# Kernel tuning notes

Hardware: AMD Instinct MI355X
Metric: run time of the kernel (lower is better)

The kernel has to match this reference:

```python
import jax, jax.numpy as jnp
import numpy as np

B, F, U, G = 2048, 512, 512, 64
REG_STRENGTH = 1.0


def setup_inputs() -> dict:
    key = jax.random.key(0)
    k0, k1, k2, k3, k4 = jax.random.split(key, 5)
    x = jax.random.normal(k0, (B, F), dtype=jnp.float32)
    gid = jax.random.randint(k1, (B,), 0, G, dtype=jnp.int64)
    # glorot-normal-ish scale for kernels: sqrt(2/(fan_in+fan_out))
    glorot = np.sqrt(2.0 / (U + F)).astype(np.float32)
    w_mu = jax.random.normal(k2, (G, U, F), dtype=jnp.float32) * glorot
    b_mu = jax.random.normal(k3, (G, U), dtype=jnp.float32) * 0.05  # 'random_normal' init
    w0_mu = jax.random.normal(k4, (U, F), dtype=jnp.float32) * glorot
    b0_mu = jnp.zeros((U,), dtype=jnp.float32)
    return {"x": x, "gid": gid, "w_mu": w_mu, "b_mu": b_mu, "w0_mu": w0_mu, "b0_mu": b0_mu}


def reference(x, gid, w_mu, b_mu, w0_mu, b0_mu):
    # Hard top-1 routing: per-sample weight matrix gather, [B, U, F]
    w = jnp.take(w_mu, gid, axis=0)
    b = jnp.take(b_mu, gid, axis=0)  # [B, U]
    # Batched matvec: 'Bup,Bp->Bu'
    outputs = jnp.einsum("buf,bf->bu", w, x) + b  # use_bias=True, activation=None
    # L2 prior regularization loss (added via add_loss in the original)
    w_loss = jnp.sum(jnp.square(w - w0_mu[None]))  # sum over axes [1,2] then batch
    b_loss = jnp.sum(jnp.square(b - b0_mu[None]))
    reg_loss = REG_STRENGTH * (w_loss + b_loss)
    return outputs, reg_loss
```

## Files before the change

kernel.cpp:

```cpp
#include <hip/hip_runtime.h>

#define B_SZ 2048
#define F_SZ 512
#define U_SZ 512
#define G_SZ 64
#define REG_STRENGTH 1.0f

#define NT 8
#define BN 64
#define BK 64
#define NSTEP (F_SZ / BK)
#define MROWS 64
#define THREADS 256
#define NBLOCKS (NT * G_SZ)

typedef float f32x4 __attribute__((ext_vector_type(4)));
typedef __bf16 bf16x8 __attribute__((ext_vector_type(8)));

#define MFMA(a, b, c) __builtin_amdgcn_mfma_f32_16x16x32_bf16((a), (b), (c), 0, 0, 0)

static __device__ __forceinline__ unsigned short bf16_rne(float f) {
  unsigned u = __float_as_uint(f);
  return (unsigned short)((u + 0x7fffu + ((u >> 16) & 1u)) >> 16);
}

static __device__ __forceinline__ void cvt8(const f32x4 a, const f32x4 b,
                                            bf16x8& h, bf16x8& l) {
#pragma unroll
  for (int i = 0; i < 4; ++i) {
    const unsigned short hb = bf16_rne(a[i]);
    h[i] = __builtin_bit_cast(__bf16, hb);
    l[i] = __builtin_bit_cast(
        __bf16, bf16_rne(a[i] - __uint_as_float((unsigned)hb << 16)));
  }
#pragma unroll
  for (int i = 0; i < 4; ++i) {
    const unsigned short hb = bf16_rne(b[i]);
    h[4 + i] = __builtin_bit_cast(__bf16, hb);
    l[4 + i] = __builtin_bit_cast(
        __bf16, bf16_rne(b[i] - __uint_as_float((unsigned)hb << 16)));
  }
}

static __device__ __forceinline__ void writeX(unsigned short* __restrict__ xh,
                                              unsigned short* __restrict__ xl,
                                              int row, int kq, const f32x4 v) {
  int byte = (row << 7) + (kq << 3);
  byte ^= (row & 7) << 4;
  const unsigned short h0 = bf16_rne(v[0]);
  const unsigned short h1 = bf16_rne(v[1]);
  const unsigned short h2 = bf16_rne(v[2]);
  const unsigned short h3 = bf16_rne(v[3]);
  const ushort4 hv = make_ushort4(h0, h1, h2, h3);
  const ushort4 lv = make_ushort4(
      bf16_rne(v[0] - __uint_as_float((unsigned)h0 << 16)),
      bf16_rne(v[1] - __uint_as_float((unsigned)h1 << 16)),
      bf16_rne(v[2] - __uint_as_float((unsigned)h2 << 16)),
      bf16_rne(v[3] - __uint_as_float((unsigned)h3 << 16)));
  *(ushort4*)((char*)xh + byte) = hv;
  *(ushort4*)((char*)xl + byte) = lv;
}

static __device__ __forceinline__ bf16x8 readA(
    const unsigned short* __restrict__ base, int m, int kk, int llo, int lhi) {
  const int row = (m << 4) + llo;
  int byte = (row << 7) + (kk << 6) + (lhi << 4);
  byte ^= (row & 7) << 4;
  return *(const bf16x8*)((const char*)base + byte);
}

__global__ __launch_bounds__(THREADS, 2) void fused_kernel(
    const float* __restrict__ x, const int* __restrict__ gid,
    const float* __restrict__ w_mu, const float* __restrict__ b_mu,
    const float* __restrict__ w0_mu, const float* __restrict__ b0_mu,
    float* __restrict__ out, float* __restrict__ wsf,
    unsigned* __restrict__ done) {
  __shared__ __align__(16) unsigned short XH[2][MROWS * BK];
  __shared__ __align__(16) unsigned short XL[2][MROWS * BK];
  __shared__ int rows_s[B_SZ];
  __shared__ int cnt_s;
  __shared__ float red_s[THREADS / 64];

  const int f = blockIdx.x;
  const int r8 = f & 7;
  const int q = f >> 3;
  const int nt = q & 7;
  const int g = ((q >> 3) << 3) + r8;

  const int tid = threadIdx.x;
  const int lane = tid & 63;
  const int wv = tid >> 6;
  const int lhi = lane >> 4;
  const int llo = lane & 15;

  if (tid == 0) cnt_s = 0;
  __syncthreads();
#pragma unroll
  for (int u = 0; u < 2; ++u) {
    const int4 v = ((const int4*)gid)[tid + u * THREADS];
    const int b0 = (tid + u * THREADS) << 2;
    if (v.x == g) rows_s[atomicAdd(&cnt_s, 1)] = b0;
    if (v.y == g) rows_s[atomicAdd(&cnt_s, 1)] = b0 + 1;
    if (v.z == g) rows_s[atomicAdd(&cnt_s, 1)] = b0 + 2;
    if (v.w == g) rows_s[atomicAdd(&cnt_s, 1)] = b0 + 3;
  }
  __syncthreads();
  const int cnt = cnt_s;

  if (cnt > 0) {
    const int mycol = nt * BN + wv * 16 + llo;
    const float* __restrict__ wrow =
        w_mu + (size_t)g * (U_SZ * F_SZ) + (size_t)mycol * F_SZ;
    const float* __restrict__ w0row = w0_mu + (size_t)mycol * F_SZ;

    float regp = 0.0f;
    if (nt == 0) {
      for (int u = tid; u < U_SZ; u += THREADS) {
        const float d = b_mu[(g << 9) + u] - b0_mu[u];
        regp += d * d;
      }
    }

    for (int r0c = 0; r0c < cnt; r0c += MROWS) {
      const int rc = min(MROWS, cnt - r0c);
      const int nf4 = rc << 4;
      const int mt = (rc + 15) >> 4;
      const bool doreg = (r0c == 0);
      f32x4 acc[4];
#pragma unroll
      for (int m = 0; m < 4; ++m) acc[m] = (f32x4){0.f, 0.f, 0.f, 0.f};

#pragma unroll
      for (int u = 0; u < 4; ++u) {
        const int i = tid + u * THREADS;
        if (i < nf4) {
          const int row = i >> 4, kq = i & 15;
          const f32x4 v = *(const f32x4*)(
              x + (size_t)rows_s[r0c + row] * F_SZ + (kq << 2));
          writeX(&XH[0][0], &XL[0][0], row, kq, v);
        }
      }
      __syncthreads();

      for (int s = 0; s < NSTEP; ++s) {
        const int buf = s & 1;
        f32x4 xr[4];
        if (s + 1 < NSTEP) {
          const int kc = (s + 1) * BK;
#pragma unroll
          for (int u = 0; u < 4; ++u) {
            const int i = tid + u * THREADS;
            if (i < nf4) {
              const int row = i >> 4, kq = i & 15;
              xr[u] = *(const f32x4*)(
                  x + (size_t)rows_s[r0c + row] * F_SZ + kc + (kq << 2));
            }
          }
        }
        const int kcs = s * BK + (lhi << 3);
        const f32x4 wa0 = *(const f32x4*)(wrow + kcs);
        const f32x4 wa1 = *(const f32x4*)(wrow + kcs + 4);
        const f32x4 wb0 = *(const f32x4*)(wrow + kcs + 32);
        const f32x4 wb1 = *(const f32x4*)(wrow + kcs + 32 + 4);
        if (doreg) {
          const f32x4 z0 = *(const f32x4*)(w0row + kcs);
          const f32x4 z1 = *(const f32x4*)(w0row + kcs + 4);
          const f32x4 z2 = *(const f32x4*)(w0row + kcs + 32);
          const f32x4 z3 = *(const f32x4*)(w0row + kcs + 32 + 4);
#pragma unroll
          for (int i = 0; i < 4; ++i) {
            const float d0 = wa0[i] - z0[i], d1 = wa1[i] - z1[i];
            const float d2 = wb0[i] - z2[i], d3 = wb1[i] - z3[i];
            regp += d0 * d0 + d1 * d1 + d2 * d2 + d3 * d3;
          }
        }
        bf16x8 wh0, wl0, wh1, wl1;
        cvt8(wa0, wa1, wh0, wl0);
        cvt8(wb0, wb1, wh1, wl1);
#pragma unroll
        for (int m = 0; m < 4; ++m) {
          if (m < mt) {
            const bf16x8 ah0 = readA(&XH[buf][0], m, 0, llo, lhi);
            const bf16x8 al0 = readA(&XL[buf][0], m, 0, llo, lhi);
            acc[m] = MFMA(ah0, wh0, acc[m]);
            acc[m] = MFMA(ah0, wl0, acc[m]);
            acc[m] = MFMA(al0, wh0, acc[m]);
            const bf16x8 ah1 = readA(&XH[buf][0], m, 1, llo, lhi);
            const bf16x8 al1 = readA(&XL[buf][0], m, 1, llo, lhi);
            acc[m] = MFMA(ah1, wh1, acc[m]);
            acc[m] = MFMA(ah1, wl1, acc[m]);
            acc[m] = MFMA(al1, wh1, acc[m]);
          }
        }
        if (s + 1 < NSTEP) {
#pragma unroll
          for (int u = 0; u < 4; ++u) {
            const int i = tid + u * THREADS;
            if (i < nf4) {
              const int row = i >> 4, kq = i & 15;
              writeX(&XH[buf ^ 1][0], &XL[buf ^ 1][0], row, kq, xr[u]);
            }
          }
        }
        __syncthreads();
      }

      const float bias = b_mu[(g << 9) + mycol];
#pragma unroll
      for (int m = 0; m < 4; ++m) {
        if (m < mt) {
#pragma unroll
          for (int j = 0; j < 4; ++j) {
            const int rl = (m << 4) + (lhi << 2) + j;
            if (rl < rc) {
              out[(size_t)rows_s[r0c + rl] * U_SZ + mycol] = acc[m][j] + bias;
            }
          }
        }
      }
    }

#pragma unroll
    for (int o = 32; o > 0; o >>= 1) regp += __shfl_down(regp, o, 64);
    if (lane == 0) red_s[wv] = regp;
    __syncthreads();
    if (tid == 0) {
      atomicAdd(wsf, (float)cnt * (red_s[0] + red_s[1] + red_s[2] + red_s[3]));
    }
  }

  if (tid == 0) {
    __threadfence();
    const unsigned prev = atomicAdd(done, 1u);
    if (prev == (unsigned)(gridDim.x - 1)) {
      __threadfence();
      const float v = atomicAdd(wsf, 0.0f);
      out[(size_t)B_SZ * U_SZ] = REG_STRENGTH * v;
    }
  }
}

extern "C" void kernel_launch(void* const* d_in, const int* in_sizes, int n_in,
                              void* d_out, int out_size, void* d_ws,
                              size_t ws_size, hipStream_t stream) {
  (void)in_sizes; (void)n_in; (void)out_size; (void)ws_size;
  const float* x     = (const float*)d_in[0];
  const int*   gid   = (const int*)d_in[1];
  const float* w_mu  = (const float*)d_in[2];
  const float* b_mu  = (const float*)d_in[3];
  const float* w0_mu = (const float*)d_in[4];
  const float* b0_mu = (const float*)d_in[5];

  float* wsf = (float*)d_ws;
  unsigned* done = (unsigned*)d_ws + 1;

  hipMemsetAsync(d_ws, 0, 8, stream);
  fused_kernel<<<NBLOCKS, THREADS, 0, stream>>>(x, gid, w_mu, b_mu, w0_mu,
                                                b0_mu, (float*)d_out, wsf, done);
}
```

Baseline: 146.0 us.

## Drop LDS staging of x; load activations straight from global per wave

Removes the double-buffered shared-memory staging of the x rows and the block-wide barriers. Each wave now loads its own x fragments directly from global memory and converts them to split bf16 in registers. Conversions use native __bf16 casts instead of manual rounding. The final reduction moves to per-wave atomics with a wave-level completion counter. This cuts LDS traffic and synchronization, but every wave reloads and reconverts the same x rows, so redundant global loads and conversion work increase.

New measurement: 192.9 us. +32.1%, slower.

```diff
diff --git a/kernel.cpp b/kernel.cpp
--- a/kernel.cpp
+++ b/kernel.cpp
@@ -7,66 +7,29 @@
 #define REG_STRENGTH 1.0f
 
 #define NT 8
-#define BN 64
-#define BK 64
-#define NSTEP (F_SZ / BK)
-#define MROWS 64
 #define THREADS 256
 #define NBLOCKS (NT * G_SZ)
+#define NWAVES (NBLOCKS * 4)
 
 typedef float f32x4 __attribute__((ext_vector_type(4)));
 typedef __bf16 bf16x8 __attribute__((ext_vector_type(8)));
 
 #define MFMA(a, b, c) __builtin_amdgcn_mfma_f32_16x16x32_bf16((a), (b), (c), 0, 0, 0)
 
-static __device__ __forceinline__ unsigned short bf16_rne(float f) {
-  unsigned u = __float_as_uint(f);
-  return (unsigned short)((u + 0x7fffu + ((u >> 16) & 1u)) >> 16);
-}
-
 static __device__ __forceinline__ void cvt8(const f32x4 a, const f32x4 b,
                                             bf16x8& h, bf16x8& l) {
 #pragma unroll
   for (int i = 0; i < 4; ++i) {
-    const unsigned short hb = bf16_rne(a[i]);
-    h[i] = __builtin_bit_cast(__bf16, hb);
-    l[i] = __builtin_bit_cast(
-        __bf16, bf16_rne(a[i] - __uint_as_float((unsigned)hb << 16)));
+    const __bf16 hb = (__bf16)a[i];
+    h[i] = hb;
+    l[i] = (__bf16)(a[i] - (float)hb);
   }
 #pragma unroll
   for (int i = 0; i < 4; ++i) {
-    const unsigned short hb = bf16_rne(b[i]);
-    h[4 + i] = __builtin_bit_cast(__bf16, hb);
-    l[4 + i] = __builtin_bit_cast(
-        __bf16, bf16_rne(b[i] - __uint_as_float((unsigned)hb << 16)));
+    const __bf16 hb = (__bf16)b[i];
+    h[4 + i] = hb;
+    l[4 + i] = (__bf16)(b[i] - (float)hb);
   }
-}
-
-static __device__ __forceinline__ void writeX(unsigned short* __restrict__ xh,
-                                              unsigned short* __restrict__ xl,
-                                              int row, int kq, const f32x4 v) {
-  int byte = (row << 7) + (kq << 3);
-  byte ^= (row & 7) << 4;
-  const unsigned short h0 = bf16_rne(v[0]);
-  const unsigned short h1 = bf16_rne(v[1]);
-  const unsigned short h2 = bf16_rne(v[2]);
-  const unsigned short h3 = bf16_rne(v[3]);
-  const ushort4 hv = make_ushort4(h0, h1, h2, h3);
-  const ushort4 lv = make_ushort4(
-      bf16_rne(v[0] - __uint_as_float((unsigned)h0 << 16)),
-      bf16_rne(v[1] - __uint_as_float((unsigned)h1 << 16)),
-      bf16_rne(v[2] - __uint_as_float((unsigned)h2 << 16)),
-      bf16_rne(v[3] - __uint_as_float((unsigned)h3 << 16)));
-  *(ushort4*)((char*)xh + byte) = hv;
-  *(ushort4*)((char*)xl + byte) = lv;
-}
-
-static __device__ __forceinline__ bf16x8 readA(
-    const unsigned short* __restrict__ base, int m, int kk, int llo, int lhi) {
-  const int row = (m << 4) + llo;
-  int byte = (row << 7) + (kk << 6) + (lhi << 4);
-  byte ^= (row & 7) << 4;
-  return *(const bf16x8*)((const char*)base + byte);
 }
 
 __global__ __launch_bounds__(THREADS, 2) void fused_kernel(
@@ -75,11 +38,8 @@
     const float* __restrict__ w0_mu, const float* __restrict__ b0_mu,
     float* __restrict__ out, float* __restrict__ wsf,
     unsigned* __restrict__ done) {
-  __shared__ __align__(16) unsigned short XH[2][MROWS * BK];
-  __shared__ __align__(16) unsigned short XL[2][MROWS * BK];
   __shared__ int rows_s[B_SZ];
   __shared__ int cnt_s;
-  __shared__ float red_s[THREADS / 64];
 
   const int f = blockIdx.x;
   const int r8 = f & 7;
@@ -108,10 +68,10 @@
   const int cnt = cnt_s;
 
   if (cnt > 0) {
-    const int mycol = nt * BN + wv * 16 + llo;
-    const float* __restrict__ wrow =
-        w_mu + (size_t)g * (U_SZ * F_SZ) + (size_t)mycol * F_SZ;
-    const float* __restrict__ w0row = w0_mu + (size_t)mycol * F_SZ;
+    const int mycol = nt * 64 + wv * 16 + llo;
+    const float* __restrict__ wp =
+        w_mu + (size_t)g * (U_SZ * F_SZ) + (size_t)mycol * F_SZ + (lhi << 3);
+    const float* __restrict__ w0p = w0_mu + (size_t)mycol * F_SZ + (lhi << 3);
 
     float regp = 0.0f;
     if (nt == 0) {
@@ -121,88 +81,50 @@
       }
     }
 
-    for (int r0c = 0; r0c < cnt; r0c += MROWS) {
-      const int rc = min(MROWS, cnt - r0c);
-      const int nf4 = rc << 4;
+    for (int r0c = 0; r0c < cnt; r0c += 64) {
+      const int rc = min(64, cnt - r0c);
       const int mt = (rc + 15) >> 4;
       const bool doreg = (r0c == 0);
+
+      const float* xp[4];
+#pragma unroll
+      for (int m = 0; m < 4; ++m) {
+        int r = r0c + (m << 4) + llo;
+        if (r >= cnt) r = cnt - 1;
+        xp[m] = x + (size_t)rows_s[r] * F_SZ + (lhi << 3);
+      }
+
       f32x4 acc[4];
 #pragma unroll
       for (int m = 0; m < 4; ++m) acc[m] = (f32x4){0.f, 0.f, 0.f, 0.f};
 
+#pragma unroll 4
+      for (int kc = 0; kc < F_SZ; kc += 32) {
+        const f32x4 wa = *(const f32x4*)(wp + kc);
+        const f32x4 wb = *(const f32x4*)(wp + kc + 4);
+        if (doreg) {
+          const f32x4 za = *(const f32x4*)(w0p + kc);
+          const f32x4 zb = *(const f32x4*)(w0p + kc + 4);
 #pragma unroll
-      for (int u = 0; u < 4; ++u) {
-        const int i = tid + u * THREADS;
-        if (i < nf4) {
-          const int row = i >> 4, kq = i & 15;
-          const f32x4 v = *(const f32x4*)(
-              x + (size_t)rows_s[r0c + row] * F_SZ + (kq << 2));
-          writeX(&XH[0][0], &XL[0][0], row, kq, v);
-        }
-      }
-      __syncthreads();
-
-      for (int s = 0; s < NSTEP; ++s) {
-        const int buf = s & 1;
-        f32x4 xr[4];
-        if (s + 1 < NSTEP) {
-          const int kc = (s + 1) * BK;
-#pragma unroll
-          for (int u = 0; u < 4; ++u) {
-            const int i = tid + u * THREADS;
-            if (i < nf4) {
-              const int row = i >> 4, kq = i & 15;
-              xr[u] = *(const f32x4*)(
-                  x + (size_t)rows_s[r0c + row] * F_SZ + kc + (kq << 2));
-            }
+          for (int i = 0; i < 4; ++i) {
+            const float d0 = wa[i] - za[i], d1 = wb[i] - zb[i];
+            regp += d0 * d0 + d1 * d1;
           }
         }
-        const int kcs = s * BK + (lhi << 3);
-        const f32x4 wa0 = *(const f32x4*)(wrow + kcs);
-        const f32x4 wa1 = *(const f32x4*)(wrow + kcs + 4);
-        const f32x4 wb0 = *(const f32x4*)(wrow + kcs + 32);
-        const f32x4 wb1 = *(const f32x4*)(wrow + kcs + 32 + 4);
-        if (doreg) {
-          const f32x4 z0 = *(const f32x4*)(w0row + kcs);
-          const f32x4 z1 = *(const f32x4*)(w0row + kcs + 4);
-          const f32x4 z2 = *(const f32x4*)(w0row + kcs + 32);
-          const f32x4 z3 = *(const f32x4*)(w0row + kcs + 32 + 4);
-#pragma unroll
-          for (int i = 0; i < 4; ++i) {
-            const float d0 = wa0[i] - z0[i], d1 = wa1[i] - z1[i];
-            const float d2 = wb0[i] - z2[i], d3 = wb1[i] - z3[i];
-            regp += d0 * d0 + d1 * d1 + d2 * d2 + d3 * d3;
-          }
-        }
-        bf16x8 wh0, wl0, wh1, wl1;
-        cvt8(wa0, wa1, wh0, wl0);
-        cvt8(wb0, wb1, wh1, wl1);
+        bf16x8 wh, wl;
+        cvt8(wa, wb, wh, wl);
 #pragma unroll
         for (int m = 0; m < 4; ++m) {
           if (m < mt) {
-            const bf16x8 ah0 = readA(&XH[buf][0], m, 0, llo, lhi);
-            const bf16x8 al0 = readA(&XL[buf][0], m, 0, llo, lhi);
-            acc[m] = MFMA(ah0, wh0, acc[m]);
-            acc[m] = MFMA(ah0, wl0, acc[m]);
-            acc[m] = MFMA(al0, wh0, acc[m]);
-            const bf16x8 ah1 = readA(&XH[buf][0], m, 1, llo, lhi);
-            const bf16x8 al1 = readA(&XL[buf][0], m, 1, llo, lhi);
-            acc[m] = MFMA(ah1, wh1, acc[m]);
-            acc[m] = MFMA(ah1, wl1, acc[m]);
-            acc[m] = MFMA(al1, wh1, acc[m]);
+            const f32x4 a0 = *(const f32x4*)(xp[m] + kc);
+            const f32x4 a1 = *(const f32x4*)(xp[m] + kc + 4);
+            bf16x8 ah, al;
+            cvt8(a0, a1, ah, al);
+            acc[m] = MFMA(ah, wh, acc[m]);
+            acc[m] = MFMA(ah, wl, acc[m]);
+            acc[m] = MFMA(al, wh, acc[m]);
           }
         }
-        if (s + 1 < NSTEP) {
-#pragma unroll
-          for (int u = 0; u < 4; ++u) {
-            const int i = tid + u * THREADS;
-            if (i < nf4) {
-              const int row = i >> 4, kq = i & 15;
-              writeX(&XH[buf ^ 1][0], &XL[buf ^ 1][0], row, kq, xr[u]);
-            }
-          }
-        }
-        __syncthreads();
       }
 
       const float bias = b_mu[(g << 9) + mycol];
@@ -222,18 +144,13 @@
 
 #pragma unroll
     for (int o = 32; o > 0; o >>= 1) regp += __shfl_down(regp, o, 64);
-    if (lane == 0) red_s[wv] = regp;
-    __syncthreads();
-    if (tid == 0) {
-      atomicAdd(wsf, (float)cnt * (red_s[0] + red_s[1] + red_s[2] + red_s[3]));
-    }
+    if (lane == 0) atomicAdd(wsf, (float)cnt * regp);
   }
 
-  if (tid == 0) {
+  if (lane == 0) {
     __threadfence();
     const unsigned prev = atomicAdd(done, 1u);
-    if (prev == (unsigned)(gridDim.x - 1)) {
-      __threadfence();
+    if (prev == (unsigned)(NWAVES - 1)) {
       const float v = atomicAdd(wsf, 0.0f);
       out[(size_t)B_SZ * U_SZ] = REG_STRENGTH * v;
     }
```
